# Kernel tuning notes

Hardware: AMD Instinct MI355X
Metric: run time of the kernel (lower is better)

## Reference

```python
import jax, jax.numpy as jnp
import numpy as np

BN_EPS = 1e-5


def _interpolate(xyz1, xyz2, points2):
    # squared pairwise distances [B, N, S]
    d = (jnp.sum(xyz1 ** 2, -1)[:, :, None]
         + jnp.sum(xyz2 ** 2, -1)[:, None, :]
         - 2.0 * jnp.einsum('bnc,bsc->bns', xyz1, xyz2))
    # 3 smallest distances (torch does a full sort; top-3 is the same math)
    neg_d, idx = jax.lax.top_k(-d, 3)          # [B, N, 3]
    dists = -neg_d
    w = 1.0 / (dists + 1e-8)
    w = w / jnp.sum(w, -1, keepdims=True)
    # gather points2 features at idx: [B, N, 3, D]
    gathered = jnp.take_along_axis(points2[:, None, :, :],
                                   idx[:, :, :, None], axis=2)
    return jnp.sum(gathered * w[:, :, :, None], axis=2)  # [B, N, D]


def _conv_bn_relu(x, w, b, gamma, beta):
    # x: [B, N, Cin]; 1x1 Conv1d == per-point dense layer
    y = jnp.einsum('bnc,oc->bno', x, w) + b
    mean = jnp.mean(y, axis=(0, 1))
    var = jnp.mean((y - mean) ** 2, axis=(0, 1))  # biased var (torch BN training)
    y = (y - mean) * jax.lax.rsqrt(var + BN_EPS) * gamma + beta
    return jax.nn.relu(y)


def setup_inputs() -> dict:
    key = jax.random.key(0)
    ks = jax.random.split(key, 8)
    B, N, S, D1, D2 = 8, 8192, 2048, 128, 256
    in_ch, mlp = D1 + D2, [256, 128]
    inp = {
        'xyz1': jax.random.normal(ks[0], (B, N, 3), jnp.float32),
        'xyz2': jax.random.normal(ks[1], (B, S, 3), jnp.float32),
        'points1': jax.random.normal(ks[2], (B, N, D1), jnp.float32),
        'points2': jax.random.normal(ks[3], (B, S, D2), jnp.float32),
    }
    c = in_ch
    for i, o in enumerate(mlp):
        kw = jax.random.fold_in(ks[4], i)
        inp[f'w{i}'] = jax.random.normal(kw, (o, c), jnp.float32) * (1.0 / np.sqrt(c))
        inp[f'b{i}'] = jnp.zeros((o,), jnp.float32)
        inp[f'g{i}'] = jnp.ones((o,), jnp.float32)
        inp[f'beta{i}'] = jnp.zeros((o,), jnp.float32)
        c = o
    return inp


def reference(xyz1, xyz2, points1, points2,
              w0, b0, g0, beta0, w1, b1, g1, beta1):
    interp = _interpolate(xyz1, xyz2, points2)          # [B, N, D2]
    x = jnp.concatenate([points1, interp], axis=-1)     # [B, N, D1+D2]
    x = _conv_bn_relu(x, w0, b0, g0, beta0)
    x = _conv_bn_relu(x, w1, b1, g1, beta1)
    return x                                            # [B, N, mlp[-1]]
```

## Files before the change

### kernel.cpp

```cpp
#include <hip/hip_runtime.h>
#include <hip/hip_bf16.h>

#define BATCH 8
#define NPTS  8192
#define SPTS  2048
#define D1C   128
#define D2C   256
#define C_IN  384
#define O0    256
#define O1    128
#define MROWS (BATCH * NPTS)
#define NCHUNK 8
#define CHSZ   256

typedef __attribute__((ext_vector_type(8))) short short8v;
typedef __attribute__((ext_vector_type(4))) float f32x4;

__device__ __forceinline__ unsigned short f2bf(float f) {
    union { float f; unsigned u; } v; v.f = f;
    unsigned u = v.u;
    return (unsigned short)((u + 0x7fffu + ((u >> 16) & 1u)) >> 16);
}
__device__ __forceinline__ float bf2f(unsigned short h) {
    union { unsigned u; float f; } v; v.u = ((unsigned)h) << 16;
    return v.f;
}
__device__ __forceinline__ void gload_lds16(const void* g, void* l) {
    __builtin_amdgcn_global_load_lds(
        (const __attribute__((address_space(1))) void*)g,
        (__attribute__((address_space(3))) void*)l, 16, 0, 0);
}

__global__ __launch_bounds__(256, 8) void nn3_scan(
    const float* __restrict__ xyz1, const float* __restrict__ xyz2,
    float* __restrict__ candD, int* __restrict__ candI)
{
    __shared__ float4 P[CHSZ];
    const int t  = threadIdx.x;
    const int qb = blockIdx.x;
    const int c  = blockIdx.y;
    const int b  = qb >> 5;

    {
        const float* src = xyz2 + ((size_t)b * SPTS + c * CHSZ) * 3;
        float px = src[t * 3 + 0];
        float py = src[t * 3 + 1];
        float pz = src[t * 3 + 2];
        P[t] = make_float4(px, py, pz, px * px + py * py + pz * pz);
    }
    __syncthreads();

    const int q = qb * 256 + t;
    const float* qp = xyz1 + (size_t)q * 3;
    const float qx = qp[0], qy = qp[1], qz = qp[2];
    const float qn = qx * qx + qy * qy + qz * qz;

    float d0 = 1e30f, d1 = 1e30f, d2 = 1e30f;
    int   i0 = 0,     i1 = 0,     i2 = 0;
    const int gbase = c * CHSZ;

    #pragma unroll 4
    for (int s = 0; s < CHSZ; ++s) {
        float4 p = P[s];
        float dot = qx * p.x + qy * p.y + qz * p.z;
        float d = (qn + p.w) - 2.0f * dot;
        bool c0 = d < d0, c1 = d < d1, c2 = d < d2;
        int gi = gbase + s;
        float t2 = __builtin_amdgcn_fmed3f(d, d1, d2);
        float t1 = __builtin_amdgcn_fmed3f(d, d0, d1);
        i2 = c1 ? i1 : (c2 ? gi : i2);
        i1 = c0 ? i0 : (c1 ? gi : i1);
        i0 = c0 ? gi : i0;
        d2 = t2; d1 = t1; d0 = fminf(d, d0);
    }

    const size_t base = (size_t)c * (MROWS * 3) + (size_t)q * 3;
    candD[base + 0] = d0; candD[base + 1] = d1; candD[base + 2] = d2;
    candI[base + 0] = i0; candI[base + 1] = i1; candI[base + 2] = i2;
}

__global__ __launch_bounds__(256) void nn3_merge(
    const float* __restrict__ candD, const int* __restrict__ candI,
    int* __restrict__ idx3, float* __restrict__ wgt3)
{
    const int q = blockIdx.x * 256 + threadIdx.x;

    float d0 = 1e30f, d1 = 1e30f, d2 = 1e30f;
    int   i0 = 0,     i1 = 0,     i2 = 0;

    #pragma unroll
    for (int c = 0; c < NCHUNK; ++c) {
        const size_t base = (size_t)c * (MROWS * 3) + (size_t)q * 3;
        #pragma unroll
        for (int j = 0; j < 3; ++j) {
            float d = candD[base + j];
            int  gi = candI[base + j];
            bool c0 = d < d0, c1 = d < d1, c2 = d < d2;
            float t2 = __builtin_amdgcn_fmed3f(d, d1, d2);
            float t1 = __builtin_amdgcn_fmed3f(d, d0, d1);
            i2 = c1 ? i1 : (c2 ? gi : i2);
            i1 = c0 ? i0 : (c1 ? gi : i1);
            i0 = c0 ? gi : i0;
            d2 = t2; d1 = t1; d0 = fminf(d, d0);
        }
    }

    float wa = 1.0f / (d0 + 1e-8f);
    float wb = 1.0f / (d1 + 1e-8f);
    float wc = 1.0f / (d2 + 1e-8f);
    float inv = 1.0f / (wa + wb + wc);
    wa *= inv; wb *= inv; wc *= inv;

    idx3[q * 3 + 0] = i0;
    idx3[q * 3 + 1] = i1;
    idx3[q * 3 + 2] = i2;
    wgt3[q * 3 + 0] = wa;
    wgt3[q * 3 + 1] = wb;
    wgt3[q * 3 + 2] = wc;
}

__global__ __launch_bounds__(256) void cvt_f32_bf16(
    const float* __restrict__ src, unsigned short* __restrict__ dst)
{
    int i = blockIdx.x * 256 + threadIdx.x;
    float4 v = ((const float4*)src)[i];
    ushort4 o;
    o.x = f2bf(v.x); o.y = f2bf(v.y); o.z = f2bf(v.z); o.w = f2bf(v.w);
    ((ushort4*)dst)[i] = o;
}

__global__ __launch_bounds__(512) void gemm0_mfma(
    const float* __restrict__ points1, const float* __restrict__ points2,
    const int* __restrict__ idx3, const float* __restrict__ wgt3,
    const unsigned short* __restrict__ w0bf, const float* __restrict__ b0,
    unsigned short* __restrict__ y0bf,
    float* __restrict__ sum0, float* __restrict__ sq0)
{
    __shared__ __align__(16) unsigned short As[128 * 32];
    __shared__ __align__(16) unsigned short Bs[256 * 32];

    const int t    = threadIdx.x;
    const int lane = t & 63;
    const int w    = t >> 6;
    const int wm   = w >> 2;
    const int wn   = w & 3;
    const int rowBase = blockIdx.x * 128;
    const int b = rowBase >> 13;

    const int r      = t >> 2;
    const int ks_log = (t & 3) ^ ((t >> 3) & 3);
    const int row_g  = rowBase + r;
    const float* p1row = points1 + (size_t)row_g * D1C;
    const float* p2b   = points2 + (size_t)b * SPTS * D2C;
    const int   gi0 = idx3[row_g * 3 + 0];
    const int   gi1 = idx3[row_g * 3 + 1];
    const int   gi2 = idx3[row_g * 3 + 2];
    const float gw0 = wgt3[row_g * 3 + 0];
    const float gw1 = wgt3[row_g * 3 + 1];
    const float gw2 = wgt3[row_g * 3 + 2];
    const float* g0p = p2b + (size_t)gi0 * D2C;
    const float* g1p = p2b + (size_t)gi1 * D2C;
    const float* g2p = p2b + (size_t)gi2 * D2C;
    unsigned short* asw = As + t * 8;

    const unsigned short* gB0 = w0bf + (size_t)r * C_IN + ks_log * 8;
    const unsigned short* gB1 = w0bf + (size_t)(128 + r) * C_IN + ks_log * 8;
    char* ldsB0 = (char*)Bs + w * 1024;
    char* ldsB1 = (char*)Bs + 8192 + w * 1024;

    const int rp = (lane & 15) * 64 + (((lane >> 4) ^ ((lane >> 1) & 3)) * 16);
    const char* aBase = (const char*)As + (wm * 64) * 64 + rp;
    const char* bBase = (const char*)Bs + (wn * 64) * 64 + rp;

    f32x4 acc[4][4] = {};

    for (int kt = 0; kt < C_IN / 32; ++kt) {
        gload_lds16(gB0 + kt * 32, ldsB0);
        gload_lds16(gB1 + kt * 32, ldsB1);
        const int k = kt * 32 + ks_log * 8;
        float4 f0, f1;
        if (kt * 32 < D1C) {
            f0 = *(const float4*)(p1row + k);
            f1 = *(const float4*)(p1row + k + 4);
        } else {
            const int k2 = k - D1C;
            float4 A0 = *(const float4*)(g0p + k2);
            float4 A1 = *(const float4*)(g0p + k2 + 4);
            float4 B0 = *(const float4*)(g1p + k2);
            float4 B1 = *(const float4*)(g1p + k2 + 4);
            float4 C0 = *(const float4*)(g2p + k2);
            float4 C1 = *(const float4*)(g2p + k2 + 4);
            f0.x = gw0 * A0.x + gw1 * B0.x + gw2 * C0.x;
            f0.y = gw0 * A0.y + gw1 * B0.y + gw2 * C0.y;
            f0.z = gw0 * A0.z + gw1 * B0.z + gw2 * C0.z;
            f0.w = gw0 * A0.w + gw1 * B0.w + gw2 * C0.w;
            f1.x = gw0 * A1.x + gw1 * B1.x + gw2 * C1.x;
            f1.y = gw0 * A1.y + gw1 * B1.y + gw2 * C1.y;
            f1.z = gw0 * A1.z + gw1 * B1.z + gw2 * C1.z;
            f1.w = gw0 * A1.w + gw1 * B1.w + gw2 * C1.w;
        }
        short8v av;
        av[0] = (short)f2bf(f0.x); av[1] = (short)f2bf(f0.y);
        av[2] = (short)f2bf(f0.z); av[3] = (short)f2bf(f0.w);
        av[4] = (short)f2bf(f1.x); av[5] = (short)f2bf(f1.y);
        av[6] = (short)f2bf(f1.z); av[7] = (short)f2bf(f1.w);
        *(short8v*)asw = av;

        __syncthreads();

        short8v a[4], bf[4];
        #pragma unroll
        for (int m = 0; m < 4; ++m) a[m]  = *(const short8v*)(aBase + m * 1024);
        #pragma unroll
        for (int n = 0; n < 4; ++n) bf[n] = *(const short8v*)(bBase + n * 1024);
        #pragma unroll
        for (int m = 0; m < 4; ++m)
            #pragma unroll
            for (int n = 0; n < 4; ++n)
                acc[m][n] = __builtin_amdgcn_mfma_f32_16x16x32_bf16(
                    a[m], bf[n], acc[m][n], 0, 0, 0);

        __syncthreads();
    }

    const int colw = wn * 64 + (lane & 15);
    const int rowE = rowBase + wm * 64 + ((lane >> 4) * 4);
    float bias[4];
    #pragma unroll
    for (int n = 0; n < 4; ++n) bias[n] = b0[colw + n * 16];

    float cs[4] = {0.f, 0.f, 0.f, 0.f}, cq[4] = {0.f, 0.f, 0.f, 0.f};
    #pragma unroll
    for (int m = 0; m < 4; ++m)
        #pragma unroll
        for (int n = 0; n < 4; ++n)
            #pragma unroll
            for (int j = 0; j < 4; ++j) {
                float v = acc[m][n][j] + bias[n];
                y0bf[(size_t)(rowE + m * 16 + j) * O0 + colw + n * 16] = f2bf(v);
                cs[n] += v; cq[n] += v * v;
            }

    #pragma unroll
    for (int n = 0; n < 4; ++n) {
        float s = cs[n], qv = cq[n];
        s  += __shfl_xor(s, 16);  s  += __shfl_xor(s, 32);
        qv += __shfl_xor(qv, 16); qv += __shfl_xor(qv, 32);
        if (lane < 16) {
            atomicAdd(&sum0[colw + n * 16], s);
            atomicAdd(&sq0[colw + n * 16], qv);
        }
    }
}

__global__ void stats_kernel(const float* __restrict__ sum, const float* __restrict__ sq,
                             const float* __restrict__ g, const float* __restrict__ beta,
                             float* __restrict__ scale, float* __restrict__ shift,
                             int C, float invM)
{
    int c = blockIdx.x * blockDim.x + threadIdx.x;
    if (c < C) {
        float mean = sum[c] * invM;
        float var  = sq[c] * invM - mean * mean;
        float s = g[c] * rsqrtf(var + 1e-5f);
        scale[c] = s;
        shift[c] = beta[c] - mean * s;
    }
}

__global__ __launch_bounds__(256) void gemm1_mfma(
    const unsigned short* __restrict__ x1, const unsigned short* __restrict__ w1bf,
    const float* __restrict__ scale0, const float* __restrict__ shift0,
    const float* __restrict__ b1, float* __restrict__ out,
    float* __restrict__ sum1, float* __restrict__ sq1)
{
    __shared__ __align__(16) unsigned short As[128 * 32];
    __shared__ __align__(16) unsigned short Bs[128 * 32];
    __shared__ float sc[O0], sh[O0];

    const int t    = threadIdx.x;
    const int lane = t & 63;
    const int w    = t >> 6;
    const int wm   = w >> 1, wn = w & 1;
    const int rowBase = blockIdx.x * 128;

    sc[t] = scale0[t];
    sh[t] = shift0[t];
    __syncthreads();

    const int r      = t >> 2;
    const int kl     = t & 3;
    const int kp     = kl ^ ((r >> 1) & 3);
    const int ks_log = kl ^ ((r >> 1) & 3);

    const unsigned short* gA0 = x1 + (size_t)(rowBase + r) * O0 + kl * 8;
    const unsigned short* gA1 = x1 + (size_t)(rowBase + 64 + r) * O0 + kl * 8;
    unsigned short* dA0 = As + r * 32 + kp * 8;
    unsigned short* dA1 = As + (64 + r) * 32 + kp * 8;

    const unsigned short* gB0 = w1bf + (size_t)r * O0 + ks_log * 8;
    const unsigned short* gB1 = w1bf + (size_t)(64 + r) * O0 + ks_log * 8;
    char* ldsB0 = (char*)Bs + w * 1024;
    char* ldsB1 = (char*)Bs + 4096 + w * 1024;

    const int rp = (lane & 15) * 64 + (((lane >> 4) ^ ((lane >> 1) & 3)) * 16);
    const char* aBase = (const char*)As + (wm * 64) * 64 + rp;
    const char* bBase = (const char*)Bs + (wn * 64) * 64 + rp;

    f32x4 acc[4][4] = {};

    for (int kt = 0; kt < O0 / 32; ++kt) {
        gload_lds16(gB0 + kt * 32, ldsB0);
        gload_lds16(gB1 + kt * 32, ldsB1);

        const int ch = kt * 32 + kl * 8;
        float4 s0v = *(const float4*)(sc + ch);
        float4 s1v = *(const float4*)(sc + ch + 4);
        float4 h0v = *(const float4*)(sh + ch);
        float4 h1v = *(const float4*)(sh + ch + 4);
        short8v v0 = *(const short8v*)(gA0 + kt * 32);
        short8v v1 = *(const short8v*)(gA1 + kt * 32);
        short8v o0, o1;
        o0[0] = (short)f2bf(fmaxf(0.f, bf2f((unsigned short)v0[0]) * s0v.x + h0v.x));
        o0[1] = (short)f2bf(fmaxf(0.f, bf2f((unsigned short)v0[1]) * s0v.y + h0v.y));
        o0[2] = (short)f2bf(fmaxf(0.f, bf2f((unsigned short)v0[2]) * s0v.z + h0v.z));
        o0[3] = (short)f2bf(fmaxf(0.f, bf2f((unsigned short)v0[3]) * s0v.w + h0v.w));
        o0[4] = (short)f2bf(fmaxf(0.f, bf2f((unsigned short)v0[4]) * s1v.x + h1v.x));
        o0[5] = (short)f2bf(fmaxf(0.f, bf2f((unsigned short)v0[5]) * s1v.y + h1v.y));
        o0[6] = (short)f2bf(fmaxf(0.f, bf2f((unsigned short)v0[6]) * s1v.z + h1v.z));
        o0[7] = (short)f2bf(fmaxf(0.f, bf2f((unsigned short)v0[7]) * s1v.w + h1v.w));
        o1[0] = (short)f2bf(fmaxf(0.f, bf2f((unsigned short)v1[0]) * s0v.x + h0v.x));
        o1[1] = (short)f2bf(fmaxf(0.f, bf2f((unsigned short)v1[1]) * s0v.y + h0v.y));
        o1[2] = (short)f2bf(fmaxf(0.f, bf2f((unsigned short)v1[2]) * s0v.z + h0v.z));
        o1[3] = (short)f2bf(fmaxf(0.f, bf2f((unsigned short)v1[3]) * s0v.w + h0v.w));
        o1[4] = (short)f2bf(fmaxf(0.f, bf2f((unsigned short)v1[4]) * s1v.x + h1v.x));
        o1[5] = (short)f2bf(fmaxf(0.f, bf2f((unsigned short)v1[5]) * s1v.y + h1v.y));
        o1[6] = (short)f2bf(fmaxf(0.f, bf2f((unsigned short)v1[6]) * s1v.z + h1v.z));
        o1[7] = (short)f2bf(fmaxf(0.f, bf2f((unsigned short)v1[7]) * s1v.w + h1v.w));
        *(short8v*)dA0 = o0;
        *(short8v*)dA1 = o1;

        __syncthreads();

        short8v a[4], bf[4];
        #pragma unroll
        for (int m = 0; m < 4; ++m) a[m]  = *(const short8v*)(aBase + m * 1024);
        #pragma unroll
        for (int n = 0; n < 4; ++n) bf[n] = *(const short8v*)(bBase + n * 1024);
        #pragma unroll
        for (int m = 0; m < 4; ++m)
            #pragma unroll
            for (int n = 0; n < 4; ++n)
                acc[m][n] = __builtin_amdgcn_mfma_f32_16x16x32_bf16(
                    a[m], bf[n], acc[m][n], 0, 0, 0);

        __syncthreads();
    }

    const int colw = wn * 64 + (lane & 15);
    const int rowE = rowBase + wm * 64 + ((lane >> 4) * 4);
    float bias[4];
    #pragma unroll
    for (int n = 0; n < 4; ++n) bias[n] = b1[colw + n * 16];

    float cs[4] = {0.f, 0.f, 0.f, 0.f}, cq[4] = {0.f, 0.f, 0.f, 0.f};
    #pragma unroll
    for (int m = 0; m < 4; ++m)
        #pragma unroll
        for (int n = 0; n < 4; ++n)
            #pragma unroll
            for (int j = 0; j < 4; ++j) {
                float v = acc[m][n][j] + bias[n];
                out[(size_t)(rowE + m * 16 + j) * O1 + colw + n * 16] = v;
                cs[n] += v; cq[n] += v * v;
            }

    #pragma unroll
    for (int n = 0; n < 4; ++n) {
        float s = cs[n], qv = cq[n];
        s  += __shfl_xor(s, 16);  s  += __shfl_xor(s, 32);
        qv += __shfl_xor(qv, 16); qv += __shfl_xor(qv, 32);
        if (lane < 16) {
            atomicAdd(&sum1[colw + n * 16], s);
            atomicAdd(&sq1[colw + n * 16], qv);
        }
    }
}

__global__ __launch_bounds__(256) void bn_relu_kernel(
    float* __restrict__ out,
    const float* __restrict__ scale, const float* __restrict__ shift)
{
    int i = blockIdx.x * blockDim.x + threadIdx.x;
    float4 v = ((float4*)out)[i];
    int c = (i * 4) & (O1 - 1);
    v.x = fmaxf(0.f, v.x * scale[c + 0] + shift[c + 0]);
    v.y = fmaxf(0.f, v.y * scale[c + 1] + shift[c + 1]);
    v.z = fmaxf(0.f, v.z * scale[c + 2] + shift[c + 2]);
    v.w = fmaxf(0.f, v.w * scale[c + 3] + shift[c + 3]);
    ((float4*)out)[i] = v;
}

extern "C" void kernel_launch(void* const* d_in, const int* in_sizes, int n_in,
                              void* d_out, int out_size, void* d_ws, size_t ws_size,
                              hipStream_t stream)
{
    const float* xyz1    = (const float*)d_in[0];
    const float* xyz2    = (const float*)d_in[1];
    const float* points1 = (const float*)d_in[2];
    const float* points2 = (const float*)d_in[3];
    const float* w0      = (const float*)d_in[4];
    const float* b0      = (const float*)d_in[5];
    const float* g0      = (const float*)d_in[6];
    const float* beta0   = (const float*)d_in[7];
    const float* w1      = (const float*)d_in[8];
    const float* b1      = (const float*)d_in[9];
    const float* g1      = (const float*)d_in[10];
    const float* beta1   = (const float*)d_in[11];

    float* wsf = (float*)d_ws;
    float* sum0   = wsf;
    float* sq0    = wsf + 256;
    float* sum1   = wsf + 512;
    float* sq1    = wsf + 640;
    float* scale0 = wsf + 768;
    float* shift0 = wsf + 1024;
    float* scale1 = wsf + 1280;
    float* shift1 = wsf + 1408;
    int*   idx3   = (int*)(wsf + 1536);
    float* wgt3   = wsf + 1536 + 3 * MROWS;
    float* candD  = wgt3 + 3 * MROWS;
    int*   candI  = (int*)(candD + 3 * NCHUNK * MROWS);
    unsigned short* w0bf = (unsigned short*)(candI + 3 * NCHUNK * MROWS);
    unsigned short* w1bf = w0bf + O0 * C_IN;
    unsigned short* y0bf = w1bf + O1 * O0;

    hipMemsetAsync(d_ws, 0, 768 * sizeof(float), stream);

    nn3_scan<<<dim3(MROWS / 256, NCHUNK), 256, 0, stream>>>(xyz1, xyz2, candD, candI);
    nn3_merge<<<MROWS / 256, 256, 0, stream>>>(candD, candI, idx3, wgt3);

    cvt_f32_bf16<<<(O0 * C_IN / 4) / 256, 256, 0, stream>>>(w0, w0bf);
    cvt_f32_bf16<<<(O1 * O0 / 4) / 256, 256, 0, stream>>>(w1, w1bf);

    gemm0_mfma<<<MROWS / 128, 512, 0, stream>>>(
        points1, points2, idx3, wgt3, w0bf, b0, y0bf, sum0, sq0);

    stats_kernel<<<1, 256, 0, stream>>>(sum0, sq0, g0, beta0, scale0, shift0,
                                        O0, 1.0f / MROWS);

    gemm1_mfma<<<MROWS / 128, 256, 0, stream>>>(
        y0bf, w1bf, scale0, shift0, b1, (float*)d_out, sum1, sq1);

    stats_kernel<<<1, 128, 0, stream>>>(sum1, sq1, g1, beta1, scale1, shift1,
                                        O1, 1.0f / MROWS);

    bn_relu_kernel<<<(out_size / 4) / 256, 256, 0, stream>>>(
        (float*)d_out, scale1, shift1);
}
```

Before: 190.6 us.

## Split interpolation gather into separate kernel producing bf16 features for GEMM0

Moves the 3-NN weighted gather of points2 out of the GEMM0 main loop into a dedicated interp_kernel that writes a bf16 interpolated feature matrix. GEMM0 then streams that matrix into LDS with direct global-to-LDS loads instead of doing three scattered float4 gathers plus FMA and conversion inside the K loop. The aim is to take irregular gather latency off the MFMA critical path, at the cost of an extra kernel launch and a round trip of a 32 MB bf16 intermediate through memory. The workspace layout is also reshuffled so y0bf aliases idx3/wgt3, which are dead by the time GEMM0 writes.

```diff
diff --git a/kernel.cpp b/kernel.cpp
--- a/kernel.cpp
+++ b/kernel.cpp
@@ -129,9 +129,38 @@
     ((ushort4*)dst)[i] = o;
 }
 
+__global__ __launch_bounds__(256) void interp_kernel(
+    const float* __restrict__ points2,
+    const int* __restrict__ idx3, const float* __restrict__ wgt3,
+    unsigned short* __restrict__ xI)
+{
+    const int w    = threadIdx.x >> 6;
+    const int lane = threadIdx.x & 63;
+    const int m    = blockIdx.x * 4 + w;
+    const int b    = m >> 13;
+
+    const float* p2b = points2 + (size_t)b * SPTS * D2C;
+    const int  gi0 = idx3[m * 3 + 0];
+    const int  gi1 = idx3[m * 3 + 1];
+    const int  gi2 = idx3[m * 3 + 2];
+    const float w0 = wgt3[m * 3 + 0];
+    const float w1 = wgt3[m * 3 + 1];
+    const float w2 = wgt3[m * 3 + 2];
+
+    float4 a = *(const float4*)(p2b + (size_t)gi0 * D2C + lane * 4);
+    float4 bb = *(const float4*)(p2b + (size_t)gi1 * D2C + lane * 4);
+    float4 c = *(const float4*)(p2b + (size_t)gi2 * D2C + lane * 4);
+
+    ushort4 o;
+    o.x = f2bf(w0 * a.x + w1 * bb.x + w2 * c.x);
+    o.y = f2bf(w0 * a.y + w1 * bb.y + w2 * c.y);
+    o.z = f2bf(w0 * a.z + w1 * bb.z + w2 * c.z);
+    o.w = f2bf(w0 * a.w + w1 * bb.w + w2 * c.w);
+    *(ushort4*)(xI + (size_t)m * D2C + lane * 4) = o;
+}
+
 __global__ __launch_bounds__(512) void gemm0_mfma(
-    const float* __restrict__ points1, const float* __restrict__ points2,
-    const int* __restrict__ idx3, const float* __restrict__ wgt3,
+    const float* __restrict__ points1, const unsigned short* __restrict__ xI,
     const unsigned short* __restrict__ w0bf, const float* __restrict__ b0,
     unsigned short* __restrict__ y0bf,
     float* __restrict__ sum0, float* __restrict__ sq0)
@@ -145,23 +174,14 @@
     const int wm   = w >> 2;
     const int wn   = w & 3;
     const int rowBase = blockIdx.x * 128;
-    const int b = rowBase >> 13;
 
     const int r      = t >> 2;
     const int ks_log = (t & 3) ^ ((t >> 3) & 3);
-    const int row_g  = rowBase + r;
-    const float* p1row = points1 + (size_t)row_g * D1C;
-    const float* p2b   = points2 + (size_t)b * SPTS * D2C;
-    const int   gi0 = idx3[row_g * 3 + 0];
-    const int   gi1 = idx3[row_g * 3 + 1];
-    const int   gi2 = idx3[row_g * 3 + 2];
-    const float gw0 = wgt3[row_g * 3 + 0];
-    const float gw1 = wgt3[row_g * 3 + 1];
-    const float gw2 = wgt3[row_g * 3 + 2];
-    const float* g0p = p2b + (size_t)gi0 * D2C;
-    const float* g1p = p2b + (size_t)gi1 * D2C;
-    const float* g2p = p2b + (size_t)gi2 * D2C;
+
+    const float* p1row = points1 + (size_t)(rowBase + r) * D1C;
+    const unsigned short* xrow = xI + (size_t)(rowBase + r) * D2C + ks_log * 8;
     unsigned short* asw = As + t * 8;
+    char* ldsA = (char*)As + w * 1024;
 
     const unsigned short* gB0 = w0bf + (size_t)r * C_IN + ks_log * 8;
     const unsigned short* gB1 = w0bf + (size_t)(128 + r) * C_IN + ks_log * 8;
@@ -177,34 +197,20 @@
     for (int kt = 0; kt < C_IN / 32; ++kt) {
         gload_lds16(gB0 + kt * 32, ldsB0);
         gload_lds16(gB1 + kt * 32, ldsB1);
-        const int k = kt * 32 + ks_log * 8;
-        float4 f0, f1;
-        if (kt * 32 < D1C) {
-            f0 = *(const float4*)(p1row + k);
-            f1 = *(const float4*)(p1row + k + 4);
+
+        if (kt < 4) {
+            const int k = kt * 32 + ks_log * 8;
+            float4 f0 = *(const float4*)(p1row + k);
+            float4 f1 = *(const float4*)(p1row + k + 4);
+            short8v av;
+            av[0] = (short)f2bf(f0.x); av[1] = (short)f2bf(f0.y);
+            av[2] = (short)f2bf(f0.z); av[3] = (short)f2bf(f0.w);
+            av[4] = (short)f2bf(f1.x); av[5] = (short)f2bf(f1.y);
+            av[6] = (short)f2bf(f1.z); av[7] = (short)f2bf(f1.w);
+            *(short8v*)asw = av;
         } else {
-            const int k2 = k - D1C;
-            float4 A0 = *(const float4*)(g0p + k2);
-            float4 A1 = *(const float4*)(g0p + k2 + 4);
-            float4 B0 = *(const float4*)(g1p + k2);
-            float4 B1 = *(const float4*)(g1p + k2 + 4);
-            float4 C0 = *(const float4*)(g2p + k2);
-            float4 C1 = *(const float4*)(g2p + k2 + 4);
-            f0.x = gw0 * A0.x + gw1 * B0.x + gw2 * C0.x;
-            f0.y = gw0 * A0.y + gw1 * B0.y + gw2 * C0.y;
-            f0.z = gw0 * A0.z + gw1 * B0.z + gw2 * C0.z;
-            f0.w = gw0 * A0.w + gw1 * B0.w + gw2 * C0.w;
-            f1.x = gw0 * A1.x + gw1 * B1.x + gw2 * C1.x;
-            f1.y = gw0 * A1.y + gw1 * B1.y + gw2 * C1.y;
-            f1.z = gw0 * A1.z + gw1 * B1.z + gw2 * C1.z;
-            f1.w = gw0 * A1.w + gw1 * B1.w + gw2 * C1.w;
+            gload_lds16(xrow + (kt - 4) * 32, ldsA);
         }
-        short8v av;
-        av[0] = (short)f2bf(f0.x); av[1] = (short)f2bf(f0.y);
-        av[2] = (short)f2bf(f0.z); av[3] = (short)f2bf(f0.w);
-        av[4] = (short)f2bf(f1.x); av[5] = (short)f2bf(f1.y);
-        av[6] = (short)f2bf(f1.z); av[7] = (short)f2bf(f1.w);
-        *(short8v*)asw = av;
 
         __syncthreads();
 
@@ -427,24 +433,27 @@
     float* shift0 = wsf + 1024;
     float* scale1 = wsf + 1280;
     float* shift1 = wsf + 1408;
-    int*   idx3   = (int*)(wsf + 1536);
-    float* wgt3   = wsf + 1536 + 3 * MROWS;
-    float* candD  = wgt3 + 3 * MROWS;
-    int*   candI  = (int*)(candD + 3 * NCHUNK * MROWS);
-    unsigned short* w0bf = (unsigned short*)(candI + 3 * NCHUNK * MROWS);
-    unsigned short* w1bf = w0bf + O0 * C_IN;
-    unsigned short* y0bf = w1bf + O1 * O0;
+    unsigned short* w0bf = (unsigned short*)(wsf + 1536);
+    unsigned short* w1bf = (unsigned short*)(wsf + 50688);
+    unsigned short* y0bf = (unsigned short*)(wsf + 67072);
+    int*   idx3   = (int*)(wsf + 67072);
+    float* wgt3   = wsf + 263680;
+    float* candD  = wsf + 460288;
+    int*   candI  = (int*)(wsf + 2033152);
+    unsigned short* xI = (unsigned short*)(wsf + 8455680);
 
     hipMemsetAsync(d_ws, 0, 768 * sizeof(float), stream);
+
+    cvt_f32_bf16<<<(O0 * C_IN / 4) / 256, 256, 0, stream>>>(w0, w0bf);
+    cvt_f32_bf16<<<(O1 * O0 / 4) / 256, 256, 0, stream>>>(w1, w1bf);
 
     nn3_scan<<<dim3(MROWS / 256, NCHUNK), 256, 0, stream>>>(xyz1, xyz2, candD, candI);
     nn3_merge<<<MROWS / 256, 256, 0, stream>>>(candD, candI, idx3, wgt3);
 
-    cvt_f32_bf16<<<(O0 * C_IN / 4) / 256, 256, 0, stream>>>(w0, w0bf);
-    cvt_f32_bf16<<<(O1 * O0 / 4) / 256, 256, 0, stream>>>(w1, w1bf);
+    interp_kernel<<<MROWS / 4, 256, 0, stream>>>(points2, idx3, wgt3, xI);
 
     gemm0_mfma<<<MROWS / 128, 512, 0, stream>>>(
-        points1, points2, idx3, wgt3, w0bf, b0, y0bf, sum0, sq0);
+        points1, xI, w0bf, b0, y0bf, sum0, sq0);
 
     stats_kernel<<<1, 256, 0, stream>>>(sum0, sq0, g0, beta0, scale0, shift0,
                                         O0, 1.0f / MROWS);
```

After: 196.2 us. 1.03x slower.
